# Performance work log

Measured on AMD Instinct MI355X. Metric: run time of the kernel, lower is better.

Reference implementation:

```python
import jax, jax.numpy as jnp
import numpy as np

B, CIN, CCTX, K, V, T, KS = 8, 512, 512, 64, 256, 1024, 23
EPS = 1e-5


def _bn(z, gamma, beta):
    # train-mode BatchNorm1d over (batch, time) per channel, biased variance
    mean = jnp.mean(z, axis=(0, 2), keepdims=True)
    var = jnp.mean((z - mean) ** 2, axis=(0, 2), keepdims=True)
    return (z - mean) * jax.lax.rsqrt(var + EPS) * gamma[None, :, None] + beta[None, :, None]


def setup_inputs() -> dict:
    key = jax.random.key(0)
    ks = jax.random.split(key, 10)
    x = jax.random.normal(ks[0], (B, CIN, T), dtype=jnp.float32)
    context = jax.random.normal(ks[1], (B, CCTX, T), dtype=jnp.float32)
    Wq = jax.random.normal(ks[2], (K, CIN), dtype=jnp.float32) * (CIN ** -0.5)
    bq = jnp.zeros((K,), dtype=jnp.float32)
    Wk = jax.random.normal(ks[3], (K, CCTX), dtype=jnp.float32) * (CCTX ** -0.5)
    bk = jnp.zeros((K,), dtype=jnp.float32)
    Wv = jax.random.normal(ks[4], (V, CCTX), dtype=jnp.float32) * (CCTX ** -0.5)
    bv = jnp.zeros((V,), dtype=jnp.float32)
    gamma_q = jnp.ones((K,), dtype=jnp.float32)
    beta_q = jnp.zeros((K,), dtype=jnp.float32)
    gamma_v = jnp.ones((V,), dtype=jnp.float32)
    beta_v = jnp.zeros((V,), dtype=jnp.float32)
    pos_w = jax.random.normal(ks[5], (K, KS), dtype=jnp.float32) * (KS ** -0.5)
    pos_b = jnp.zeros((K,), dtype=jnp.float32)
    return {"x": x, "context": context, "Wq": Wq, "bq": bq, "Wk": Wk, "bk": bk,
            "Wv": Wv, "bv": bv, "gamma_q": gamma_q, "beta_q": beta_q,
            "gamma_v": gamma_v, "beta_v": beta_v, "pos_w": pos_w, "pos_b": pos_b}


def reference(x, context, Wq, bq, Wk, bk, Wv, bv,
              gamma_q, beta_q, gamma_v, beta_v, pos_w, pos_b):
    # 1x1 conv1d == channel matmul
    queries = jnp.einsum('bct,kc->bkt', x, Wq) + bq[None, :, None]          # (B,K,T)
    keys = jnp.einsum('bct,kc->bkt', context, Wk) + bk[None, :, None]       # (B,K,T)
    values = jnp.einsum('bct,vc->bvt', context, Wv) + bv[None, :, None]     # (B,V,T)

    norm_keys = jax.nn.softmax(keys, axis=-1)                               # softmax over T
    queries = _bn(queries, gamma_q, beta_q)
    values = _bn(values, gamma_v, beta_v)

    q_t = jnp.transpose(queries, (0, 2, 1))                                 # (B,T,K)
    v_t = jnp.transpose(values, (0, 2, 1))                                  # (B,T,V)

    content_lambda = jnp.einsum('bkt,btv->bkv', norm_keys, v_t)             # (B,K,V)

    # positional conv2d: kernel (K,1,KS,1), padding (KS//2, 0) along T
    lhs = v_t[:, None, :, :]                                                # (B,1,T,V)
    rhs = pos_w[:, None, :, None]                                           # (K,1,KS,1)
    pl = jax.lax.conv_general_dilated(
        lhs, rhs, window_strides=(1, 1),
        padding=[(KS // 2, KS // 2), (0, 0)],
        dimension_numbers=('NCHW', 'OIHW', 'NCHW'))
    pl = pl + pos_b[None, :, None, None]                                    # (B,K,T,V)
    pl = jnp.transpose(pl, (0, 2, 1, 3))                                    # (B,T,K,V)

    content_out = jnp.einsum('btk,bkv->btv', q_t, content_lambda)           # (B,T,V)
    positional_out = jnp.einsum('btk,btkv->btv', q_t, pl)                   # (B,T,V)

    return jnp.transpose(content_out + positional_out, (0, 2, 1))           # (B,V,T)
```

## Files before the change

### kernel.cpp

```cpp
#include <hip/hip_runtime.h>
#include <math.h>

#define B_ 8
#define CIN_ 512
#define K_ 64
#define V_ 256
#define T_ 1024
#define KS_ 23
#define EPS_ 1e-5f
#define NTC_ 16

typedef __attribute__((ext_vector_type(8))) short bf16x8;
typedef __attribute__((ext_vector_type(4))) float f32x4;

__device__ __forceinline__ unsigned short f2bf(float f) {
    union { float f; unsigned u; } x; x.f = f;
    unsigned r = x.u + 0x7fffu + ((x.u >> 16) & 1u);
    return (unsigned short)(r >> 16);
}
__device__ __forceinline__ float bf2f(unsigned short h) {
    union { unsigned u; float f; } x; x.u = ((unsigned)h) << 16;
    return x.f;
}

__global__ __launch_bounds__(256) void prep_kernel(
    const float* __restrict__ x, const float* __restrict__ ctx,
    const float* __restrict__ Wq, const float* __restrict__ Wk,
    const float* __restrict__ Wv,
    unsigned short* __restrict__ xT, unsigned short* __restrict__ cT,
    unsigned short* __restrict__ Wb, float* __restrict__ stat)
{
    __shared__ unsigned short sh[64][72];
    const int tid = threadIdx.x;
    const int id = blockIdx.x;
    if (id < 2048) {
        const int t0 = (id & 15) * 64, c0 = ((id >> 4) & 7) * 64;
        const int z = id >> 7, b = z & 7, which = z >> 3;
        const float* src = which ? ctx : x;
        unsigned short* dst = which ? cT : xT;
        const int cl = tid >> 2, qq = tid & 3;
        const float* row = src + ((size_t)b * CIN_ + c0 + cl) * T_ + t0 + qq * 16;
        #pragma unroll
        for (int u = 0; u < 4; u++) {
            float4 f = *(const float4*)(row + 4 * u);
            sh[qq * 16 + 4 * u + 0][cl] = f2bf(f.x);
            sh[qq * 16 + 4 * u + 1][cl] = f2bf(f.y);
            sh[qq * 16 + 4 * u + 2][cl] = f2bf(f.z);
            sh[qq * 16 + 4 * u + 3][cl] = f2bf(f.w);
        }
        __syncthreads();
        const int tl = tid >> 2;
        unsigned short* orow = dst + ((size_t)b * T_ + t0 + tl) * CIN_ + c0 + qq * 16;
        *(bf16x8*)(orow)     = *(bf16x8*)&sh[tl][qq * 16];
        *(bf16x8*)(orow + 8) = *(bf16x8*)&sh[tl][qq * 16 + 8];
    } else {
        const int wid = id - 2048;
        if (wid == 0 && tid < 160)
            ((float4*)stat)[tid] = make_float4(0.f, 0.f, 0.f, 0.f);
        const int i4 = wid * 256 + tid;
        const int n1 = K_ * CIN_ / 4, n2 = 2 * K_ * CIN_ / 4;
        const float* src; int off;
        if (i4 < n1)      { src = Wq; off = i4; }
        else if (i4 < n2) { src = Wk; off = i4 - n1; }
        else              { src = Wv; off = i4 - n2; }
        float4 f = ((const float4*)src)[off];
        ushort4 h;
        h.x = f2bf(f.x); h.y = f2bf(f.y); h.z = f2bf(f.z); h.w = f2bf(f.w);
        *(ushort4*)(Wb + (size_t)i4 * 4) = h;
    }
}

__global__ __launch_bounds__(256) void proj_mfma4(
    const unsigned short* __restrict__ xT, const unsigned short* __restrict__ cT,
    const unsigned short* __restrict__ Wb,
    const float* __restrict__ bq, const float* __restrict__ bk,
    const float* __restrict__ bv,
    float* __restrict__ k_buf, float* __restrict__ v_raw,
    unsigned short* __restrict__ qT, float* __restrict__ stat,
    float* __restrict__ kml)
{
    __shared__ unsigned short Wt[64][72];
    __shared__ unsigned short Xt[128][72];
    const int tid = threadIdx.x;
    const int b = blockIdx.z, t0 = blockIdx.x * 128, yb = blockIdx.y;

    const unsigned short* in; const unsigned short* W; const float* bias;
    float* outp = nullptr; int ch0 = 0; float* ssum = nullptr; float* ssq = nullptr;
    if (yb == 0)      { in = xT; W = Wb;             bias = bq;
                        ssum = stat; ssq = stat + 64; ch0 = 0; }
    else if (yb == 1) { in = cT; W = Wb + K_ * CIN_; bias = bk;
                        outp = k_buf + (size_t)b * K_ * T_; }
    else { int m0 = (yb - 2) * 64; in = cT;
           W = Wb + 2 * K_ * CIN_ + (size_t)m0 * CIN_; bias = bv + m0;
           outp = v_raw + ((size_t)b * V_ + m0) * T_;
           ssum = stat + 128; ssq = stat + 384; ch0 = m0; }

    const int lane = tid & 63, w = tid >> 6;
    const int col = lane & 15, quad = lane >> 4;
    const int wm = tid >> 2, wp = tid & 3;
    const int xt = tid >> 1, xh = tid & 1;

    f32x4 acc[8];
    #pragma unroll
    for (int j = 0; j < 8; j++) acc[j] = (f32x4){0.f, 0.f, 0.f, 0.f};

    for (int c0 = 0; c0 < CIN_; c0 += 64) {
        {
            const unsigned short* ws = W + (size_t)wm * CIN_ + c0 + wp * 16;
            *(bf16x8*)&Wt[wm][wp * 16]     = *(const bf16x8*)(ws);
            *(bf16x8*)&Wt[wm][wp * 16 + 8] = *(const bf16x8*)(ws + 8);
            const unsigned short* xs = in + ((size_t)b * T_ + t0 + xt) * CIN_ + c0 + xh * 32;
            #pragma unroll
            for (int u = 0; u < 4; u++)
                *(bf16x8*)&Xt[xt][xh * 32 + 8 * u] = *(const bf16x8*)(xs + 8 * u);
        }
        __syncthreads();
        #pragma unroll
        for (int ks = 0; ks < 2; ks++) {
            const int kc = ks * 32 + quad * 8;
            bf16x8 af = *(bf16x8*)&Wt[w * 16 + col][kc];
            #pragma unroll
            for (int j = 0; j < 8; j++) {
                bf16x8 bfr = *(bf16x8*)&Xt[j * 16 + col][kc];
                acc[j] = __builtin_amdgcn_mfma_f32_16x16x32_bf16(af, bfr, acc[j], 0, 0, 0);
            }
        }
        __syncthreads();
    }

    float bias_v[4], s[4], sq[4], mr[4], lr[4];
    #pragma unroll
    for (int r = 0; r < 4; r++) {
        bias_v[r] = bias[w * 16 + quad * 4 + r];
        s[r] = 0.f; sq[r] = 0.f; mr[r] = -1e30f; lr[r] = 0.f;
    }
    #pragma unroll
    for (int j = 0; j < 8; j++) {
        float o[4];
        #pragma unroll
        for (int r = 0; r < 4; r++) {
            o[r] = acc[j][r] + bias_v[r];
            s[r] += o[r]; sq[r] += o[r] * o[r];
        }
        if (yb == 0) {
            ushort4 h;
            h.x = f2bf(o[0]); h.y = f2bf(o[1]); h.z = f2bf(o[2]); h.w = f2bf(o[3]);
            *(ushort4*)(qT + ((size_t)b * T_ + t0 + j * 16 + col) * K_ + w * 16 + quad * 4) = h;
        } else {
            #pragma unroll
            for (int r = 0; r < 4; r++)
                outp[(size_t)(w * 16 + quad * 4 + r) * T_ + t0 + j * 16 + col] = o[r];
            if (yb == 1) {
                #pragma unroll
                for (int r = 0; r < 4; r++) {
                    float mn = fmaxf(mr[r], o[r]);
                    lr[r] = lr[r] * __expf(mr[r] - mn) + __expf(o[r] - mn);
                    mr[r] = mn;
                }
            }
        }
    }
    if (yb == 1) {
        #pragma unroll
        for (int r = 0; r < 4; r++) {
            float m = mr[r], l = lr[r];
            #pragma unroll
            for (int off = 1; off < 16; off <<= 1) {
                float mo = __shfl_xor(m, off, 64);
                float lo = __shfl_xor(l, off, 64);
                float mn = fmaxf(m, mo);
                l = l * __expf(m - mn) + lo * __expf(mo - mn);
                m = mn;
            }
            if (col == 0) {
                int row = w * 16 + quad * 4 + r;
                float* p = kml + (((size_t)b * K_ + row) * 8 + (t0 >> 7)) * 2;
                p[0] = m; p[1] = l;
            }
        }
    } else {
        #pragma unroll
        for (int r = 0; r < 4; r++) {
            float sv = s[r], qv = sq[r];
            #pragma unroll
            for (int off = 1; off < 16; off <<= 1) {
                sv += __shfl_xor(sv, off, 64);
                qv += __shfl_xor(qv, off, 64);
            }
            if (col == 0) {
                int ch = ch0 + w * 16 + quad * 4 + r;
                atomicAdd(&ssum[ch], sv);
                atomicAdd(&ssq[ch], qv);
            }
        }
    }
}

__global__ __launch_bounds__(256) void lambda_kernel4(
    const float* __restrict__ k_buf, const float* __restrict__ v_raw,
    const float* __restrict__ kml, float* __restrict__ clp)
{
    __shared__ __align__(16) float nks[K_][68];
    __shared__ __align__(16) float vls[64][68];
    __shared__ float mrow[64], lrow[64];
    const int tid = threadIdx.x;
    const int b = blockIdx.z, v0 = blockIdx.y * 64, tc = blockIdx.x, t0 = tc * 64;

    if (tid < 64) {
        const float2* p = (const float2*)(kml + ((size_t)b * K_ + tid) * 16);
        float m = -1e30f, l = 0.f;
        #pragma unroll
        for (int sgi = 0; sgi < 8; sgi++) {
            float2 ml = p[sgi];
            float mn = fmaxf(m, ml.x);
            l = l * __expf(m - mn) + ml.y * __expf(ml.x - mn);
            m = mn;
        }
        mrow[tid] = m; lrow[tid] = 1.f / l;
    }
    __syncthreads();
    {
        const int r = tid >> 2, q = tid & 3;
        const float* nrow = k_buf + ((size_t)b * K_ + r) * T_ + t0;
        const float* vrow = v_raw + ((size_t)b * V_ + v0 + r) * T_ + t0;
        const float mr = mrow[r], li = lrow[r];
        #pragma unroll
        for (int i = 0; i < 4; i++) {
            int c4 = q + 4 * i;
            float4 g = *(const float4*)(nrow + 4 * c4);
            g.x = __expf(g.x - mr) * li; g.y = __expf(g.y - mr) * li;
            g.z = __expf(g.z - mr) * li; g.w = __expf(g.w - mr) * li;
            *(float4*)&nks[r][4 * c4] = g;
            float4 h = *(const float4*)(vrow + 4 * c4);
            vls[4 * c4 + 0][r] = h.x; vls[4 * c4 + 1][r] = h.y;
            vls[4 * c4 + 2][r] = h.z; vls[4 * c4 + 3][r] = h.w;
        }
    }
    __syncthreads();
    const int tv = tid & 15, tk = tid >> 4;
    float4 acc[4];
    #pragma unroll
    for (int i = 0; i < 4; i++) acc[i] = make_float4(0.f, 0.f, 0.f, 0.f);
    for (int tt = 0; tt < 16; tt++) {
        float4 w0 = *(float4*)&vls[4 * tt + 0][4 * tv];
        float4 w1 = *(float4*)&vls[4 * tt + 1][4 * tv];
        float4 w2 = *(float4*)&vls[4 * tt + 2][4 * tv];
        float4 w3 = *(float4*)&vls[4 * tt + 3][4 * tv];
        #pragma unroll
        for (int i = 0; i < 4; i++) {
            float4 n = *(float4*)&nks[4 * tk + i][4 * tt];
            acc[i] += w0 * n.x + w1 * n.y + w2 * n.z + w3 * n.w;
        }
    }
    #pragma unroll
    for (int i = 0; i < 4; i++)
        *(float4*)&clp[(((size_t)b * NTC_ + tc) * K_ + 4 * tk + i) * V_ + v0 + 4 * tv] = acc[i];
}

__global__ __launch_bounds__(256) void prep_cl_kernel2(
    const float* __restrict__ clp, const float* __restrict__ stat,
    const float* __restrict__ gq, const float* __restrict__ betaq,
    const float* __restrict__ gv, const float* __restrict__ betav,
    unsigned short* __restrict__ clb2, float* __restrict__ hterm)
{
    __shared__ float qsc[64], qsh[64], red[4][64];
    const int tid = threadIdx.x;
    const int b = blockIdx.y, v0 = blockIdx.x * 64;
    const float inv_n = 1.f / (B_ * T_);
    if (tid < 64) {
        float mean = stat[tid] * inv_n;
        float var  = stat[64 + tid] * inv_n - mean * mean;
        float sc = gq[tid] * rsqrtf(var + EPS_);
        qsc[tid] = sc; qsh[tid] = betaq[tid] - mean * sc;
    }
    const int vl = tid & 63, kq = tid >> 6;
    const int c = v0 + vl;
    float vmean = stat[128 + c] * inv_n;
    float vvar  = stat[384 + c] * inv_n - vmean * vmean;
    float vsv = gv[c] * rsqrtf(vvar + EPS_);
    float vhv = betav[c] - vmean * vsv;
    __syncthreads();
    float h = 0.f;
    for (int kk = 0; kk < 16; kk++) {
        int k = kq * 16 + kk;
        float a = 0.f;
        #pragma unroll
        for (int tc = 0; tc < NTC_; tc++)
            a += clp[(((size_t)b * NTC_ + tc) * K_ + k) * V_ + c];
        float clbv = a * vsv + vhv;
        h += qsh[k] * clbv;
        clb2[((size_t)b * V_ + c) * K_ + k] = f2bf(clbv * qsc[k]);
    }
    red[kq][vl] = h;
    __syncthreads();
    if (tid < 64)
        hterm[(size_t)b * V_ + v0 + tid] =
            red[0][tid] + red[1][tid] + red[2][tid] + red[3][tid];
}

__global__ __launch_bounds__(256) void out_kernel4(
    const unsigned short* __restrict__ qT, const unsigned short* __restrict__ clb2,
    const float* __restrict__ hterm, const float* __restrict__ v_raw,
    const float* __restrict__ stat,
    const float* __restrict__ gq, const float* __restrict__ betaq,
    const float* __restrict__ gv, const float* __restrict__ betav,
    const float* __restrict__ pos_w, const float* __restrict__ pos_b,
    float* __restrict__ out)
{
    __shared__ unsigned short qTt[64][72];
    __shared__ unsigned short clv[64][72];
    __shared__ float vs2T[88][68];
    __shared__ float qpt[64][24];
    __shared__ float pws[64][24];
    __shared__ float qsc[64], qsh[64];
    __shared__ float consts[24];
    __shared__ float hvs[64];
    const int tid = threadIdx.x;
    const int b = blockIdx.z, v0 = blockIdx.y * 64, t0 = blockIdx.x * 64;
    const float inv_n = 1.f / (B_ * T_);

    if (tid < 64) {
        float mean = stat[tid] * inv_n;
        float var  = stat[64 + tid] * inv_n - mean * mean;
        float sc = gq[tid] * rsqrtf(var + EPS_);
        qsc[tid] = sc; qsh[tid] = betaq[tid] - mean * sc;
        hvs[tid] = hterm[(size_t)b * V_ + v0 + tid];
    }
    {
        const int rl = tid >> 2, part = tid & 3;
        const unsigned short* qs = qT + ((size_t)b * T_ + t0 + rl) * K_ + part * 16;
        *(bf16x8*)&qTt[rl][part * 16]     = *(const bf16x8*)(qs);
        *(bf16x8*)&qTt[rl][part * 16 + 8] = *(const bf16x8*)(qs + 8);
        const unsigned short* cs = clb2 + ((size_t)b * V_ + v0 + rl) * K_ + part * 16;
        *(bf16x8*)&clv[rl][part * 16]     = *(const bf16x8*)(cs);
        *(bf16x8*)&clv[rl][part * 16 + 8] = *(const bf16x8*)(cs + 8);
    }
    {
        const int vl = tid >> 2, qq = tid & 3;
        const int c = v0 + vl;
        float vmean = stat[128 + c] * inv_n;
        float vvar  = stat[384 + c] * inv_n - vmean * vmean;
        float vsv = gv[c] * rsqrtf(vvar + EPS_);
        float vhv = betav[c] - vmean * vsv;
        const float* vrow = v_raw + ((size_t)b * V_ + c) * T_;
        #pragma unroll
        for (int i = 0; i < 22; i++) {
            int cc = qq + 4 * i;
            if (cc < 86) {
                int t = t0 + cc - 11;
                vs2T[cc][vl] = (t >= 0 && t < T_) ? vrow[t] * vsv + vhv : 0.f;
            }
        }
    }
    __syncthreads();

    for (int idx = tid; idx < K_ * 24; idx += 256) {
        int k = idx / 24, s = idx % 24;
        pws[k][s] = qsc[k] * (s < KS_ ? pos_w[k * KS_ + s] : pos_b[k]);
    }
    if (tid < 24) {
        float cs = 0.f;
        for (int k = 0; k < K_; k++)
            cs += qsh[k] * (tid < KS_ ? pos_w[k * KS_ + tid] : pos_b[k]);
        consts[tid] = cs;
    }
    __syncthreads();

    {
        const int t = tid >> 2, sg = tid & 3, s0 = sg * 6;
        float a[6];
        #pragma unroll
        for (int u = 0; u < 6; u++) a[u] = consts[s0 + u];
        #pragma unroll
        for (int kb = 0; kb < 8; kb++) {
            bf16x8 qv = *(bf16x8*)&qTt[t][kb * 8];
            #pragma unroll
            for (int j = 0; j < 8; j++) {
                float q = bf2f((unsigned short)qv[j]);
                #pragma unroll
                for (int u = 0; u < 6; u++) a[u] += q * pws[kb * 8 + j][s0 + u];
            }
        }
        #pragma unroll
        for (int u = 0; u < 6; u++) qpt[t][s0 + u] = a[u];
    }
    __syncthreads();

    const int lane = tid & 63, w = tid >> 6;
    const int col = lane & 15, quad = lane >> 4;

    f32x4 acc[4];
    #pragma unroll
    for (int tf = 0; tf < 4; tf++) acc[tf] = (f32x4){0.f, 0.f, 0.f, 0.f};

    #pragma unroll
    for (int ks = 0; ks < 2; ks++) {
        const int kc = ks * 32 + quad * 8;
        bf16x8 af = *(bf16x8*)&clv[w * 16 + col][kc];
        #pragma unroll
        for (int tf = 0; tf < 4; tf++) {
            bf16x8 bq = *(bf16x8*)&qTt[tf * 16 + col][kc];
            acc[tf] = __builtin_amdgcn_mfma_f32_16x16x32_bf16(af, bq, acc[tf], 0, 0, 0);
        }
    }

    const int vb = w * 16 + quad * 4;
    float4 hv4 = *(float4*)&hvs[vb];
    #pragma unroll
    for (int tf = 0; tf < 4; tf++) {
        const int lt = tf * 16 + col;
        float qv[24];
        #pragma unroll
        for (int u = 0; u < 6; u++)
            *(float4*)&qv[4 * u] = *(float4*)&qpt[lt][4 * u];
        float4 a; a.x = acc[tf][0]; a.y = acc[tf][1]; a.z = acc[tf][2]; a.w = acc[tf][3];
        #pragma unroll
        for (int s = 0; s < KS_; s++) {
            float4 wv = *(float4*)&vs2T[lt + s][vb];
            a.x += qv[s] * wv.x; a.y += qv[s] * wv.y;
            a.z += qv[s] * wv.z; a.w += qv[s] * wv.w;
        }
        float base = qv[23];
        a.x += base + hv4.x; a.y += base + hv4.y;
        a.z += base + hv4.z; a.w += base + hv4.w;
        float* ap = (float*)&a;
        #pragma unroll
        for (int r = 0; r < 4; r++)
            out[((size_t)b * V_ + v0 + vb + r) * T_ + t0 + lt] = ap[r];
    }
}

extern "C" void kernel_launch(void* const* d_in, const int* in_sizes, int n_in,
                              void* d_out, int out_size, void* d_ws, size_t ws_size,
                              hipStream_t stream)
{
    const float* x     = (const float*)d_in[0];
    const float* ctx   = (const float*)d_in[1];
    const float* Wq    = (const float*)d_in[2];
    const float* bq    = (const float*)d_in[3];
    const float* Wk    = (const float*)d_in[4];
    const float* bk    = (const float*)d_in[5];
    const float* Wv    = (const float*)d_in[6];
    const float* bv    = (const float*)d_in[7];
    const float* gq    = (const float*)d_in[8];
    const float* betaq = (const float*)d_in[9];
    const float* gv    = (const float*)d_in[10];
    const float* betav = (const float*)d_in[11];
    const float* pos_w = (const float*)d_in[12];
    const float* pos_b = (const float*)d_in[13];
    float* out = (float*)d_out;

    float* ws    = (float*)d_ws;
    float* k_buf = ws;
    float* v_raw = k_buf + (size_t)B_ * K_ * T_;
    float* clp   = v_raw + (size_t)B_ * V_ * T_;
    float* stat  = clp + (size_t)B_ * NTC_ * K_ * V_;
    float* hterm = stat + 640;
    float* kml   = hterm + (size_t)B_ * V_;
    unsigned short* xT   = (unsigned short*)(kml + (size_t)B_ * K_ * 16);
    unsigned short* cT   = xT + (size_t)B_ * T_ * CIN_;
    unsigned short* Wb   = cT + (size_t)B_ * T_ * CIN_;
    unsigned short* qT   = Wb + (size_t)(2 * K_ + V_) * CIN_;
    unsigned short* clb2 = qT + (size_t)B_ * T_ * K_;

    prep_kernel<<<dim3(2048 + 192), 256, 0, stream>>>(
        x, ctx, Wq, Wk, Wv, xT, cT, Wb, stat);
    proj_mfma4<<<dim3(T_ / 128, 6, B_), 256, 0, stream>>>(
        xT, cT, Wb, bq, bk, bv, k_buf, v_raw, qT, stat, kml);
    lambda_kernel4<<<dim3(NTC_, V_ / 64, B_), 256, 0, stream>>>(k_buf, v_raw, kml, clp);
    prep_cl_kernel2<<<dim3(V_ / 64, B_), 256, 0, stream>>>(
        clp, stat, gq, betaq, gv, betav, clb2, hterm);
    out_kernel4<<<dim3(T_ / 64, V_ / 64, B_), 256, 0, stream>>>(
        qT, clb2, hterm, v_raw, stat, gq, betaq, gv, betav, pos_w, pos_b, out);
}
```

Baseline: 155.6 us.

## Store keys/values as bf16 and fuse lambda reduction via last-block counter

The projection kernel now writes the key and raw value intermediates as bf16 rather than fp32, halving their write and read traffic in the lambda and output kernels. The separate prep_cl kernel is folded into the lambda kernel. The last block per (batch, v-tile) to finish, found through an atomic counter after a threadfence, does the cross-chunk reduction and BN folding. This saves one launch but lowers the precision of the values and keys. The counters are zeroed in prep_kernel by widening the stat clear.

```diff
diff --git a/kernel.cpp b/kernel.cpp
--- a/kernel.cpp
+++ b/kernel.cpp
@@ -55,7 +55,7 @@
         *(bf16x8*)(orow + 8) = *(bf16x8*)&sh[tl][qq * 16 + 8];
     } else {
         const int wid = id - 2048;
-        if (wid == 0 && tid < 160)
+        if (wid == 0 && tid < 168)
             ((float4*)stat)[tid] = make_float4(0.f, 0.f, 0.f, 0.f);
         const int i4 = wid * 256 + tid;
         const int n1 = K_ * CIN_ / 4, n2 = 2 * K_ * CIN_ / 4;
@@ -70,12 +70,12 @@
     }
 }
 
-__global__ __launch_bounds__(256) void proj_mfma4(
+__global__ __launch_bounds__(256) void proj_mfma5(
     const unsigned short* __restrict__ xT, const unsigned short* __restrict__ cT,
     const unsigned short* __restrict__ Wb,
     const float* __restrict__ bq, const float* __restrict__ bk,
     const float* __restrict__ bv,
-    float* __restrict__ k_buf, float* __restrict__ v_raw,
+    unsigned short* __restrict__ k_bufh, unsigned short* __restrict__ v_rawh,
     unsigned short* __restrict__ qT, float* __restrict__ stat,
     float* __restrict__ kml)
 {
@@ -85,14 +85,15 @@
     const int b = blockIdx.z, t0 = blockIdx.x * 128, yb = blockIdx.y;
 
     const unsigned short* in; const unsigned short* W; const float* bias;
-    float* outp = nullptr; int ch0 = 0; float* ssum = nullptr; float* ssq = nullptr;
+    unsigned short* outp = nullptr; int ch0 = 0;
+    float* ssum = nullptr; float* ssq = nullptr;
     if (yb == 0)      { in = xT; W = Wb;             bias = bq;
                         ssum = stat; ssq = stat + 64; ch0 = 0; }
     else if (yb == 1) { in = cT; W = Wb + K_ * CIN_; bias = bk;
-                        outp = k_buf + (size_t)b * K_ * T_; }
+                        outp = k_bufh + (size_t)b * K_ * T_; }
     else { int m0 = (yb - 2) * 64; in = cT;
            W = Wb + 2 * K_ * CIN_ + (size_t)m0 * CIN_; bias = bv + m0;
-           outp = v_raw + ((size_t)b * V_ + m0) * T_;
+           outp = v_rawh + ((size_t)b * V_ + m0) * T_;
            ssum = stat + 128; ssq = stat + 384; ch0 = m0; }
 
     const int lane = tid & 63, w = tid >> 6;
@@ -149,7 +150,7 @@
         } else {
             #pragma unroll
             for (int r = 0; r < 4; r++)
-                outp[(size_t)(w * 16 + quad * 4 + r) * T_ + t0 + j * 16 + col] = o[r];
+                outp[(size_t)(w * 16 + quad * 4 + r) * T_ + t0 + j * 16 + col] = f2bf(o[r]);
             if (yb == 1) {
                 #pragma unroll
                 for (int r = 0; r < 4; r++) {
@@ -196,13 +197,19 @@
     }
 }
 
-__global__ __launch_bounds__(256) void lambda_kernel4(
-    const float* __restrict__ k_buf, const float* __restrict__ v_raw,
-    const float* __restrict__ kml, float* __restrict__ clp)
+__global__ __launch_bounds__(256) void lambda_kernel5(
+    const unsigned short* __restrict__ k_bufh, const unsigned short* __restrict__ v_rawh,
+    const float* __restrict__ kml, float* __restrict__ clp,
+    const float* __restrict__ stat,
+    const float* __restrict__ gq, const float* __restrict__ betaq,
+    const float* __restrict__ gv, const float* __restrict__ betav,
+    unsigned short* __restrict__ clb2, float* __restrict__ hterm,
+    int* __restrict__ cnt)
 {
     __shared__ __align__(16) float nks[K_][68];
     __shared__ __align__(16) float vls[64][68];
     __shared__ float mrow[64], lrow[64];
+    __shared__ int lastdone;
     const int tid = threadIdx.x;
     const int b = blockIdx.z, v0 = blockIdx.y * 64, tc = blockIdx.x, t0 = tc * 64;
 
@@ -221,19 +228,19 @@
     __syncthreads();
     {
         const int r = tid >> 2, q = tid & 3;
-        const float* nrow = k_buf + ((size_t)b * K_ + r) * T_ + t0;
-        const float* vrow = v_raw + ((size_t)b * V_ + v0 + r) * T_ + t0;
+        const unsigned short* nrow = k_bufh + ((size_t)b * K_ + r) * T_ + t0 + q * 16;
+        const unsigned short* vrow = v_rawh + ((size_t)b * V_ + v0 + r) * T_ + t0 + q * 16;
         const float mr = mrow[r], li = lrow[r];
-        #pragma unroll
-        for (int i = 0; i < 4; i++) {
-            int c4 = q + 4 * i;
-            float4 g = *(const float4*)(nrow + 4 * c4);
-            g.x = __expf(g.x - mr) * li; g.y = __expf(g.y - mr) * li;
-            g.z = __expf(g.z - mr) * li; g.w = __expf(g.w - mr) * li;
-            *(float4*)&nks[r][4 * c4] = g;
-            float4 h = *(const float4*)(vrow + 4 * c4);
-            vls[4 * c4 + 0][r] = h.x; vls[4 * c4 + 1][r] = h.y;
-            vls[4 * c4 + 2][r] = h.z; vls[4 * c4 + 3][r] = h.w;
+        bf16x8 ka = *(const bf16x8*)(nrow);
+        bf16x8 kb = *(const bf16x8*)(nrow + 8);
+        bf16x8 va = *(const bf16x8*)(vrow);
+        bf16x8 vb = *(const bf16x8*)(vrow + 8);
+        #pragma unroll
+        for (int i = 0; i < 8; i++) {
+            nks[r][q * 16 + i]     = __expf(bf2f((unsigned short)ka[i]) - mr) * li;
+            nks[r][q * 16 + 8 + i] = __expf(bf2f((unsigned short)kb[i]) - mr) * li;
+            vls[q * 16 + i][r]     = bf2f((unsigned short)va[i]);
+            vls[q * 16 + 8 + i][r] = bf2f((unsigned short)vb[i]);
         }
     }
     __syncthreads();
@@ -255,17 +262,18 @@
     #pragma unroll
     for (int i = 0; i < 4; i++)
         *(float4*)&clp[(((size_t)b * NTC_ + tc) * K_ + 4 * tk + i) * V_ + v0 + 4 * tv] = acc[i];
-}
-
-__global__ __launch_bounds__(256) void prep_cl_kernel2(
-    const float* __restrict__ clp, const float* __restrict__ stat,
-    const float* __restrict__ gq, const float* __restrict__ betaq,
-    const float* __restrict__ gv, const float* __restrict__ betav,
-    unsigned short* __restrict__ clb2, float* __restrict__ hterm)
-{
+
+    __threadfence();
+    __syncthreads();
+    if (tid == 0) {
+        int old = atomicAdd(&cnt[b * 4 + (v0 >> 6)], 1);
+        lastdone = (old == NTC_ - 1);
+    }
+    __syncthreads();
+    if (!lastdone) return;
+    __threadfence();
+
     __shared__ float qsc[64], qsh[64], red[4][64];
-    const int tid = threadIdx.x;
-    const int b = blockIdx.y, v0 = blockIdx.x * 64;
     const float inv_n = 1.f / (B_ * T_);
     if (tid < 64) {
         float mean = stat[tid] * inv_n;
@@ -285,8 +293,8 @@
         int k = kq * 16 + kk;
         float a = 0.f;
         #pragma unroll
-        for (int tc = 0; tc < NTC_; tc++)
-            a += clp[(((size_t)b * NTC_ + tc) * K_ + k) * V_ + c];
+        for (int t2 = 0; t2 < NTC_; t2++)
+            a += clp[(((size_t)b * NTC_ + t2) * K_ + k) * V_ + c];
         float clbv = a * vsv + vhv;
         h += qsh[k] * clbv;
         clb2[((size_t)b * V_ + c) * K_ + k] = f2bf(clbv * qsc[k]);
@@ -298,9 +306,9 @@
             red[0][tid] + red[1][tid] + red[2][tid] + red[3][tid];
 }
 
-__global__ __launch_bounds__(256) void out_kernel4(
+__global__ __launch_bounds__(256) void out_kernel5(
     const unsigned short* __restrict__ qT, const unsigned short* __restrict__ clb2,
-    const float* __restrict__ hterm, const float* __restrict__ v_raw,
+    const float* __restrict__ hterm, const unsigned short* __restrict__ v_rawh,
     const float* __restrict__ stat,
     const float* __restrict__ gq, const float* __restrict__ betaq,
     const float* __restrict__ gv, const float* __restrict__ betav,
@@ -342,13 +350,13 @@
         float vvar  = stat[384 + c] * inv_n - vmean * vmean;
         float vsv = gv[c] * rsqrtf(vvar + EPS_);
         float vhv = betav[c] - vmean * vsv;
-        const float* vrow = v_raw + ((size_t)b * V_ + c) * T_;
+        const unsigned short* vrow = v_rawh + ((size_t)b * V_ + c) * T_;
         #pragma unroll
         for (int i = 0; i < 22; i++) {
             int cc = qq + 4 * i;
             if (cc < 86) {
                 int t = t0 + cc - 11;
-                vs2T[cc][vl] = (t >= 0 && t < T_) ? vrow[t] * vsv + vhv : 0.f;
+                vs2T[cc][vl] = (t >= 0 && t < T_) ? bf2f(vrow[t]) * vsv + vhv : 0.f;
             }
         }
     }
@@ -451,25 +459,25 @@
     float* out = (float*)d_out;
 
     float* ws    = (float*)d_ws;
-    float* k_buf = ws;
-    float* v_raw = k_buf + (size_t)B_ * K_ * T_;
-    float* clp   = v_raw + (size_t)B_ * V_ * T_;
+    float* clp   = ws;
     float* stat  = clp + (size_t)B_ * NTC_ * K_ * V_;
-    float* hterm = stat + 640;
+    int*   cnt   = (int*)(stat + 640);
+    float* hterm = stat + 672;
     float* kml   = hterm + (size_t)B_ * V_;
-    unsigned short* xT   = (unsigned short*)(kml + (size_t)B_ * K_ * 16);
-    unsigned short* cT   = xT + (size_t)B_ * T_ * CIN_;
-    unsigned short* Wb   = cT + (size_t)B_ * T_ * CIN_;
-    unsigned short* qT   = Wb + (size_t)(2 * K_ + V_) * CIN_;
-    unsigned short* clb2 = qT + (size_t)B_ * T_ * K_;
+    unsigned short* k_bufh = (unsigned short*)(kml + (size_t)B_ * K_ * 16);
+    unsigned short* v_rawh = k_bufh + (size_t)B_ * K_ * T_;
+    unsigned short* xT     = v_rawh + (size_t)B_ * V_ * T_;
+    unsigned short* cT     = xT + (size_t)B_ * T_ * CIN_;
+    unsigned short* Wb     = cT + (size_t)B_ * T_ * CIN_;
+    unsigned short* qT     = Wb + (size_t)(2 * K_ + V_) * CIN_;
+    unsigned short* clb2   = qT + (size_t)B_ * T_ * K_;
 
     prep_kernel<<<dim3(2048 + 192), 256, 0, stream>>>(
         x, ctx, Wq, Wk, Wv, xT, cT, Wb, stat);
-    proj_mfma4<<<dim3(T_ / 128, 6, B_), 256, 0, stream>>>(
-        xT, cT, Wb, bq, bk, bv, k_buf, v_raw, qT, stat, kml);
-    lambda_kernel4<<<dim3(NTC_, V_ / 64, B_), 256, 0, stream>>>(k_buf, v_raw, kml, clp);
-    prep_cl_kernel2<<<dim3(V_ / 64, B_), 256, 0, stream>>>(
-        clp, stat, gq, betaq, gv, betav, clb2, hterm);
-    out_kernel4<<<dim3(T_ / 64, V_ / 64, B_), 256, 0, stream>>>(
-        qT, clb2, hterm, v_raw, stat, gq, betaq, gv, betav, pos_w, pos_b, out);
-}
+    proj_mfma5<<<dim3(T_ / 128, 6, B_), 256, 0, stream>>>(
+        xT, cT, Wb, bq, bk, bv, k_bufh, v_rawh, qT, stat, kml);
+    lambda_kernel5<<<dim3(NTC_, V_ / 64, B_), 256, 0, stream>>>(
+        k_bufh, v_rawh, kml, clp, stat, gq, betaq, gv, betav, clb2, hterm, cnt);
+    out_kernel5<<<dim3(T_ / 64, V_ / 64, B_), 256, 0, stream>>>(
+        qT, clb2, hterm, v_rawh, stat, gq, betaq, gv, betav, pos_w, pos_b, out);
+}
```

Result: slower. 221.8 us (+42.5%).
